# Optimization experiments

Hardware: AMD Instinct MI355X
Metric: run time of the kernel (lower is better)

The kernel has to match this reference:

```python
import jax, jax.numpy as jnp
import numpy as np

N = 6144
INPUT_SIZE = 1024
HIDDEN = 256
NEG_INF = -9e15  # matches torch masked_fill value -9000000000000000.0


def setup_inputs() -> dict:
    key = jax.random.key(0)
    k1, k2, k3, k4 = jax.random.split(key, 4)
    nodes_embed = jax.random.normal(k1, (N, INPUT_SIZE), dtype=jnp.float32)
    node_adj = jax.random.randint(k2, (N, N), 0, 2, dtype=jnp.int32)
    # learned params (xavier-uniform-ish scaling)
    limW = np.sqrt(6.0 / (INPUT_SIZE + HIDDEN))
    W = jax.random.uniform(k3, (INPUT_SIZE, HIDDEN), minval=-limW, maxval=limW, dtype=jnp.float32)
    lima = 1.414 * np.sqrt(6.0 / (2 * HIDDEN + 1))
    a_edge = jax.random.uniform(k4, (2 * HIDDEN,), minval=-lima, maxval=lima, dtype=jnp.float32)
    return {"nodes_embed": nodes_embed, "W": W, "a_edge": a_edge, "node_adj": node_adj}


def reference(nodes_embed, W, a_edge, node_adj):
    # h = nodes_embed @ W : [N, hidden]
    h = nodes_embed @ W
    # W_edge([h_i ; h_j]) decomposes exactly: (h_i @ a1) + (h_j @ a2)
    a1, a2 = a_edge[:HIDDEN], a_edge[HIDDEN:]
    score = (h @ a1)[:, None] + (h @ a2)[None, :]  # [N, N]
    adj_f = node_adj.astype(h.dtype)
    weight = jax.nn.leaky_relu(adj_f * score, negative_slope=0.2)
    weight = jnp.where(node_adj == 0, jnp.asarray(NEG_INF, h.dtype), weight)
    attention = jax.nn.softmax(weight, axis=-1)
    # dropout in eval mode (identity)
    return attention @ h  # [N, hidden]
```

## Files before the change

kernel.cpp:

```cpp
#include <hip/hip_runtime.h>
#include <hip/hip_bf16.h>

#define NN 6144
#define INPUT 1024
#define HID 256

using frag  = __attribute__((ext_vector_type(8))) short;
using f32x4 = __attribute__((ext_vector_type(4))) float;

static __device__ __forceinline__ unsigned short bf16u(float x) {
    unsigned u = __float_as_uint(x);
    u += 0x7fff + ((u >> 16) & 1);
    return (unsigned short)(u >> 16);
}

static __device__ __forceinline__ void lds_barrier() {
    asm volatile("s_waitcnt lgkmcnt(0)" ::: "memory");
    __builtin_amdgcn_s_barrier();
    __builtin_amdgcn_sched_barrier(0);
}

__global__ __launch_bounds__(256) void k_prep(const float* __restrict__ X,
                                              const float* __restrict__ W,
                                              unsigned short* __restrict__ Xb,
                                              unsigned short* __restrict__ Wt) {
    int b = blockIdx.x;
    if (b < 3072) {
        int t = b * 256 + threadIdx.x;
        const float4* p = reinterpret_cast<const float4*>(X) + (size_t)t * 2;
        float4 x0 = p[0], x1 = p[1];
        frag v;
        v[0] = (short)bf16u(x0.x); v[1] = (short)bf16u(x0.y);
        v[2] = (short)bf16u(x0.z); v[3] = (short)bf16u(x0.w);
        v[4] = (short)bf16u(x1.x); v[5] = (short)bf16u(x1.y);
        v[6] = (short)bf16u(x1.z); v[7] = (short)bf16u(x1.w);
        *reinterpret_cast<frag*>(Xb + (size_t)t * 8) = v;
    } else {
        int t = (b - 3072) * 256 + threadIdx.x;
        int n = t >> 10, k = t & 1023;
        Wt[t] = bf16u(W[k * HID + n]);
    }
}

__global__ __launch_bounds__(256) void k_gemm1(const unsigned short* __restrict__ Xb,
                                               const unsigned short* __restrict__ Wt,
                                               const float* __restrict__ a_edge,
                                               unsigned short* __restrict__ hT,
                                               float* __restrict__ s1,
                                               float* __restrict__ s2) {
    __shared__ unsigned short A[2][32][72];
    int t = threadIdx.x;
    int m = t >> 3, cg = t & 7;
    int i0 = blockIdx.x * 32, n0 = blockIdx.y * 64;
    int w = t >> 6, l = t & 63, lm = l & 15, q = l >> 4;
    int nw = n0 + w * 16;

    const unsigned short* xrow = Xb + (size_t)(i0 + m) * INPUT + cg * 8;
    const unsigned short* brow = Wt + (size_t)(nw + lm) * INPUT + q * 8;

    f32x4 acc0 = {}, acc1 = {};
    frag av = *reinterpret_cast<const frag*>(xrow);

    for (int c = 0; c < 16; c++) {
        int buf = c & 1;
        frag b0 = *reinterpret_cast<const frag*>(brow + c * 64);
        frag b1 = *reinterpret_cast<const frag*>(brow + c * 64 + 32);

        *reinterpret_cast<frag*>(&A[buf][m][cg * 8]) = av;
        if (c < 15) av = *reinterpret_cast<const frag*>(xrow + (c + 1) * 64);

        lds_barrier();

#pragma unroll
        for (int kk = 0; kk < 2; kk++) {
            frag a0 = *reinterpret_cast<const frag*>(&A[buf][lm][kk * 32 + q * 8]);
            frag a1 = *reinterpret_cast<const frag*>(&A[buf][16 + lm][kk * 32 + q * 8]);
            frag b  = kk ? b1 : b0;
            acc0 = __builtin_amdgcn_mfma_f32_16x16x32_bf16(a0, b, acc0, 0, 0, 0);
            acc1 = __builtin_amdgcn_mfma_f32_16x16x32_bf16(a1, b, acc1, 0, 0, 0);
        }
    }

    ushort4 o;
    o.x = bf16u(acc0[0]); o.y = bf16u(acc0[1]); o.z = bf16u(acc0[2]); o.w = bf16u(acc0[3]);
    *reinterpret_cast<ushort4*>(hT + (size_t)(nw + lm) * NN + i0 + q * 4) = o;
    o.x = bf16u(acc1[0]); o.y = bf16u(acc1[1]); o.z = bf16u(acc1[2]); o.w = bf16u(acc1[3]);
    *reinterpret_cast<ushort4*>(hT + (size_t)(nw + lm) * NN + i0 + 16 + q * 4) = o;

    float a1v = a_edge[nw + lm], a2v = a_edge[HID + nw + lm];
#pragma unroll
    for (int h = 0; h < 2; h++) {
        const f32x4& ac = h ? acc1 : acc0;
#pragma unroll
        for (int r = 0; r < 4; r++) {
            float v1 = ac[r] * a1v, v2 = ac[r] * a2v;
            v1 += __shfl_xor(v1, 1); v2 += __shfl_xor(v2, 1);
            v1 += __shfl_xor(v1, 2); v2 += __shfl_xor(v2, 2);
            v1 += __shfl_xor(v1, 4); v2 += __shfl_xor(v2, 4);
            v1 += __shfl_xor(v1, 8); v2 += __shfl_xor(v2, 8);
            if (lm == 0) {
                atomicAdd(&s1[i0 + h * 16 + q * 4 + r], v1);
                atomicAdd(&s2[i0 + h * 16 + q * 4 + r], v2);
            }
        }
    }
}

__global__ __launch_bounds__(512) void k_attn(const int* __restrict__ adj,
                                              const float* __restrict__ s1,
                                              const float* __restrict__ s2,
                                              const unsigned short* __restrict__ hT,
                                              float* __restrict__ U4,
                                              float* __restrict__ denom4) {
    __shared__ unsigned short P[2][32][136];
    int t = threadIdx.x;
    int m = t >> 4, cg = t & 15;
    int i0 = blockIdx.x * 32;
    int q4 = blockIdx.y;
    int j0 = q4 * 1536;
    int w = t >> 6, l = t & 63, lm = l & 15, q = l >> 4;

    float s1v = s1[i0 + m];
    const int*   arow = adj + (size_t)(i0 + m) * NN + j0 + cg * 8;
    const float* s2p  = s2 + j0 + cg * 8;

    const unsigned short* brow[2];
#pragma unroll
    for (int nt = 0; nt < 2; nt++)
        brow[nt] = hT + (size_t)(w * 32 + nt * 16 + lm) * NN + j0 + q * 8;

    f32x4 acc[2][2] = {};
    float dsum = 0.f;

    int4   ca0 = *reinterpret_cast<const int4*>(arow);
    int4   ca1 = *reinterpret_cast<const int4*>(arow + 4);
    float4 cs0 = *reinterpret_cast<const float4*>(s2p);
    float4 cs1 = *reinterpret_cast<const float4*>(s2p + 4);

    for (int c = 0; c < 12; c++) {
        int buf = c & 1;
        int jc = c * 128;

        frag bf[8];
#pragma unroll
        for (int kk = 0; kk < 4; kk++)
#pragma unroll
            for (int nt = 0; nt < 2; nt++)
                bf[kk * 2 + nt] = *reinterpret_cast<const frag*>(brow[nt] + jc + kk * 32);

        int4 na0 = {}, na1 = {};
        float4 ns0 = {}, ns1 = {};
        if (c < 11) {
            na0 = *reinterpret_cast<const int4*>(arow + jc + 128);
            na1 = *reinterpret_cast<const int4*>(arow + jc + 132);
            ns0 = *reinterpret_cast<const float4*>(s2p + jc + 128);
            ns1 = *reinterpret_cast<const float4*>(s2p + jc + 132);
        }

        float sc, wv, p0, p1, p2, p3, p4, p5, p6, p7;
        sc = s1v + cs0.x; wv = fmaxf(sc, 0.2f * sc); p0 = ca0.x ? __expf(wv) : 0.f;
        sc = s1v + cs0.y; wv = fmaxf(sc, 0.2f * sc); p1 = ca0.y ? __expf(wv) : 0.f;
        sc = s1v + cs0.z; wv = fmaxf(sc, 0.2f * sc); p2 = ca0.z ? __expf(wv) : 0.f;
        sc = s1v + cs0.w; wv = fmaxf(sc, 0.2f * sc); p3 = ca0.w ? __expf(wv) : 0.f;
        sc = s1v + cs1.x; wv = fmaxf(sc, 0.2f * sc); p4 = ca1.x ? __expf(wv) : 0.f;
        sc = s1v + cs1.y; wv = fmaxf(sc, 0.2f * sc); p5 = ca1.y ? __expf(wv) : 0.f;
        sc = s1v + cs1.z; wv = fmaxf(sc, 0.2f * sc); p6 = ca1.z ? __expf(wv) : 0.f;
        sc = s1v + cs1.w; wv = fmaxf(sc, 0.2f * sc); p7 = ca1.w ? __expf(wv) : 0.f;
        dsum += ((p0 + p1) + (p2 + p3)) + ((p4 + p5) + (p6 + p7));
        frag pk;
        pk[0] = (short)bf16u(p0); pk[1] = (short)bf16u(p1);
        pk[2] = (short)bf16u(p2); pk[3] = (short)bf16u(p3);
        pk[4] = (short)bf16u(p4); pk[5] = (short)bf16u(p5);
        pk[6] = (short)bf16u(p6); pk[7] = (short)bf16u(p7);
        *reinterpret_cast<frag*>(&P[buf][m][cg * 8]) = pk;

        lds_barrier();

        __builtin_amdgcn_s_setprio(1);
#pragma unroll
        for (int kk = 0; kk < 4; kk++) {
            frag a0 = *reinterpret_cast<const frag*>(&P[buf][lm][kk * 32 + q * 8]);
            frag a1 = *reinterpret_cast<const frag*>(&P[buf][16 + lm][kk * 32 + q * 8]);
#pragma unroll
            for (int nt = 0; nt < 2; nt++) {
                acc[0][nt] = __builtin_amdgcn_mfma_f32_16x16x32_bf16(a0, bf[kk * 2 + nt], acc[0][nt], 0, 0, 0);
                acc[1][nt] = __builtin_amdgcn_mfma_f32_16x16x32_bf16(a1, bf[kk * 2 + nt], acc[1][nt], 0, 0, 0);
            }
        }
        __builtin_amdgcn_s_setprio(0);

        ca0 = na0; ca1 = na1; cs0 = ns0; cs1 = ns1;
    }

    float v = dsum;
    v += __shfl_xor(v, 1); v += __shfl_xor(v, 2);
    v += __shfl_xor(v, 4); v += __shfl_xor(v, 8);
    if (cg == 0) denom4[(size_t)q4 * NN + i0 + m] = v;

    float* Ub = U4 + (size_t)q4 * NN * HID;
#pragma unroll
    for (int h = 0; h < 2; h++)
#pragma unroll
        for (int nt = 0; nt < 2; nt++)
#pragma unroll
            for (int r = 0; r < 4; r++)
                Ub[(size_t)(i0 + h * 16 + q * 4 + r) * HID + w * 32 + nt * 16 + lm] = acc[h][nt][r];
}

__global__ __launch_bounds__(256) void k_norm(const float* __restrict__ U4,
                                              const float* __restrict__ denom4,
                                              float* __restrict__ out) {
    int i = blockIdx.x, t = threadIdx.x;
    size_t S = (size_t)NN * HID;
    size_t base = (size_t)i * HID + t;
    float u = U4[base] + U4[base + S] + U4[base + 2 * S] + U4[base + 3 * S];
    float d = denom4[i] + denom4[i + NN] + denom4[i + 2 * NN] + denom4[i + 3 * NN];
    out[base] = (d != 0.f) ? u / d : 0.f;
}

extern "C" void kernel_launch(void* const* d_in, const int* in_sizes, int n_in,
                              void* d_out, int out_size, void* d_ws, size_t ws_size,
                              hipStream_t stream) {
    const float* X      = (const float*)d_in[0];
    const float* W      = (const float*)d_in[1];
    const float* a_edge = (const float*)d_in[2];
    const int*   adj    = (const int*)d_in[3];
    float* out = (float*)d_out;

    float* U4     = (float*)d_ws;
    float* denom4 = U4 + (size_t)4 * NN * HID;
    float* s1     = denom4 + (size_t)4 * NN;
    float* s2     = s1 + NN;
    unsigned short* hT = (unsigned short*)(s2 + NN);
    unsigned short* Wt = hT + (size_t)HID * NN;
    unsigned short* Xb = (unsigned short*)U4;

    hipMemsetAsync(s1, 0, 2 * NN * sizeof(float), stream);
    k_prep<<<3072 + INPUT * HID / 256, 256, 0, stream>>>(X, W, Xb, Wt);
    k_gemm1<<<dim3(NN / 32, HID / 64), 256, 0, stream>>>(Xb, Wt, a_edge, hT, s1, s2);
    k_attn<<<dim3(NN / 32, 4), 512, 0, stream>>>(adj, s1, s2, hT, U4, denom4);
    k_norm<<<NN, 256, 0, stream>>>(U4, denom4, out);
}
```

Measured before the change: 300.0 us.

## Drop LDS staging in projection GEMM, register-prefetch fragments, deepen attention adjacency prefetch

The projection GEMM now loads A and B MFMA fragments straight from global memory into double-buffered registers, with no LDS staging and no barriers. Each block runs 512 threads and covers 128 output columns. The attention kernel prefetches adjacency and s2 two chunks ahead instead of one, and both kernels get a launch-bounds occupancy hint of 4. The aim is to hide global latency better, at the cost of more registers and redundant global reads of X rows across waves.

```diff
diff --git a/kernel.cpp b/kernel.cpp
--- a/kernel.cpp
+++ b/kernel.cpp
@@ -42,52 +42,57 @@
     }
 }
 
-__global__ __launch_bounds__(256) void k_gemm1(const unsigned short* __restrict__ Xb,
-                                               const unsigned short* __restrict__ Wt,
-                                               const float* __restrict__ a_edge,
-                                               unsigned short* __restrict__ hT,
-                                               float* __restrict__ s1,
-                                               float* __restrict__ s2) {
-    __shared__ unsigned short A[2][32][72];
+__global__ __launch_bounds__(512, 4) void k_gemm1(const unsigned short* __restrict__ Xb,
+                                                  const unsigned short* __restrict__ Wt,
+                                                  const float* __restrict__ a_edge,
+                                                  unsigned short* __restrict__ hT,
+                                                  float* __restrict__ s1,
+                                                  float* __restrict__ s2) {
     int t = threadIdx.x;
-    int m = t >> 3, cg = t & 7;
-    int i0 = blockIdx.x * 32, n0 = blockIdx.y * 64;
+    int i0 = blockIdx.x * 32;
     int w = t >> 6, l = t & 63, lm = l & 15, q = l >> 4;
-    int nw = n0 + w * 16;
-
-    const unsigned short* xrow = Xb + (size_t)(i0 + m) * INPUT + cg * 8;
-    const unsigned short* brow = Wt + (size_t)(nw + lm) * INPUT + q * 8;
+    int n0 = blockIdx.y * 128 + w * 16;
+
+    const unsigned short* arow0 = Xb + (size_t)(i0 + lm) * INPUT + q * 8;
+    const unsigned short* arow1 = arow0 + 16 * INPUT;
+    const unsigned short* brow  = Wt + (size_t)(n0 + lm) * INPUT + q * 8;
 
     f32x4 acc0 = {}, acc1 = {};
-    frag av = *reinterpret_cast<const frag*>(xrow);
-
-    for (int c = 0; c < 16; c++) {
-        int buf = c & 1;
-        frag b0 = *reinterpret_cast<const frag*>(brow + c * 64);
-        frag b1 = *reinterpret_cast<const frag*>(brow + c * 64 + 32);
-
-        *reinterpret_cast<frag*>(&A[buf][m][cg * 8]) = av;
-        if (c < 15) av = *reinterpret_cast<const frag*>(xrow + (c + 1) * 64);
-
-        lds_barrier();
-
-#pragma unroll
-        for (int kk = 0; kk < 2; kk++) {
-            frag a0 = *reinterpret_cast<const frag*>(&A[buf][lm][kk * 32 + q * 8]);
-            frag a1 = *reinterpret_cast<const frag*>(&A[buf][16 + lm][kk * 32 + q * 8]);
-            frag b  = kk ? b1 : b0;
-            acc0 = __builtin_amdgcn_mfma_f32_16x16x32_bf16(a0, b, acc0, 0, 0, 0);
-            acc1 = __builtin_amdgcn_mfma_f32_16x16x32_bf16(a1, b, acc1, 0, 0, 0);
+
+    frag A0[2][4], A1[2][4], B[2][4];
+#pragma unroll
+    for (int j = 0; j < 4; j++) {
+        A0[0][j] = *reinterpret_cast<const frag*>(arow0 + j * 32);
+        A1[0][j] = *reinterpret_cast<const frag*>(arow1 + j * 32);
+        B[0][j]  = *reinterpret_cast<const frag*>(brow  + j * 32);
+    }
+
+#pragma unroll
+    for (int g = 0; g < 8; g++) {
+        int cur = g & 1, nxt = cur ^ 1;
+        if (g < 7) {
+#pragma unroll
+            for (int j = 0; j < 4; j++) {
+                int kk = (g + 1) * 4 + j;
+                A0[nxt][j] = *reinterpret_cast<const frag*>(arow0 + kk * 32);
+                A1[nxt][j] = *reinterpret_cast<const frag*>(arow1 + kk * 32);
+                B[nxt][j]  = *reinterpret_cast<const frag*>(brow  + kk * 32);
+            }
+        }
+#pragma unroll
+        for (int j = 0; j < 4; j++) {
+            acc0 = __builtin_amdgcn_mfma_f32_16x16x32_bf16(A0[cur][j], B[cur][j], acc0, 0, 0, 0);
+            acc1 = __builtin_amdgcn_mfma_f32_16x16x32_bf16(A1[cur][j], B[cur][j], acc1, 0, 0, 0);
         }
     }
 
     ushort4 o;
     o.x = bf16u(acc0[0]); o.y = bf16u(acc0[1]); o.z = bf16u(acc0[2]); o.w = bf16u(acc0[3]);
-    *reinterpret_cast<ushort4*>(hT + (size_t)(nw + lm) * NN + i0 + q * 4) = o;
+    *reinterpret_cast<ushort4*>(hT + (size_t)(n0 + lm) * NN + i0 + q * 4) = o;
     o.x = bf16u(acc1[0]); o.y = bf16u(acc1[1]); o.z = bf16u(acc1[2]); o.w = bf16u(acc1[3]);
-    *reinterpret_cast<ushort4*>(hT + (size_t)(nw + lm) * NN + i0 + 16 + q * 4) = o;
-
-    float a1v = a_edge[nw + lm], a2v = a_edge[HID + nw + lm];
+    *reinterpret_cast<ushort4*>(hT + (size_t)(n0 + lm) * NN + i0 + 16 + q * 4) = o;
+
+    float a1v = a_edge[n0 + lm], a2v = a_edge[HID + n0 + lm];
 #pragma unroll
     for (int h = 0; h < 2; h++) {
         const f32x4& ac = h ? acc1 : acc0;
@@ -106,12 +111,12 @@
     }
 }
 
-__global__ __launch_bounds__(512) void k_attn(const int* __restrict__ adj,
-                                              const float* __restrict__ s1,
-                                              const float* __restrict__ s2,
-                                              const unsigned short* __restrict__ hT,
-                                              float* __restrict__ U4,
-                                              float* __restrict__ denom4) {
+__global__ __launch_bounds__(512, 4) void k_attn(const int* __restrict__ adj,
+                                                 const float* __restrict__ s1,
+                                                 const float* __restrict__ s2,
+                                                 const unsigned short* __restrict__ hT,
+                                                 float* __restrict__ U4,
+                                                 float* __restrict__ denom4) {
     __shared__ unsigned short P[2][32][136];
     int t = threadIdx.x;
     int m = t >> 4, cg = t & 15;
@@ -136,6 +141,10 @@
     int4   ca1 = *reinterpret_cast<const int4*>(arow + 4);
     float4 cs0 = *reinterpret_cast<const float4*>(s2p);
     float4 cs1 = *reinterpret_cast<const float4*>(s2p + 4);
+    int4   na0 = *reinterpret_cast<const int4*>(arow + 128);
+    int4   na1 = *reinterpret_cast<const int4*>(arow + 132);
+    float4 ns0 = *reinterpret_cast<const float4*>(s2p + 128);
+    float4 ns1 = *reinterpret_cast<const float4*>(s2p + 132);
 
     for (int c = 0; c < 12; c++) {
         int buf = c & 1;
@@ -148,13 +157,13 @@
             for (int nt = 0; nt < 2; nt++)
                 bf[kk * 2 + nt] = *reinterpret_cast<const frag*>(brow[nt] + jc + kk * 32);
 
-        int4 na0 = {}, na1 = {};
-        float4 ns0 = {}, ns1 = {};
-        if (c < 11) {
-            na0 = *reinterpret_cast<const int4*>(arow + jc + 128);
-            na1 = *reinterpret_cast<const int4*>(arow + jc + 132);
-            ns0 = *reinterpret_cast<const float4*>(s2p + jc + 128);
-            ns1 = *reinterpret_cast<const float4*>(s2p + jc + 132);
+        int4 xa0 = {}, xa1 = {};
+        float4 xs0 = {}, xs1 = {};
+        if (c < 10) {
+            xa0 = *reinterpret_cast<const int4*>(arow + jc + 256);
+            xa1 = *reinterpret_cast<const int4*>(arow + jc + 260);
+            xs0 = *reinterpret_cast<const float4*>(s2p + jc + 256);
+            xs1 = *reinterpret_cast<const float4*>(s2p + jc + 260);
         }
 
         float sc, wv, p0, p1, p2, p3, p4, p5, p6, p7;
@@ -190,6 +199,7 @@
         __builtin_amdgcn_s_setprio(0);
 
         ca0 = na0; ca1 = na1; cs0 = ns0; cs1 = ns1;
+        na0 = xa0; na1 = xa1; ns0 = xs0; ns1 = xs1;
     }
 
     float v = dsum;
@@ -237,7 +247,7 @@
 
     hipMemsetAsync(s1, 0, 2 * NN * sizeof(float), stream);
     k_prep<<<3072 + INPUT * HID / 256, 256, 0, stream>>>(X, W, Xb, Wt);
-    k_gemm1<<<dim3(NN / 32, HID / 64), 256, 0, stream>>>(Xb, Wt, a_edge, hT, s1, s2);
+    k_gemm1<<<dim3(NN / 32, 2), 512, 0, stream>>>(Xb, Wt, a_edge, hT, s1, s2);
     k_attn<<<dim3(NN / 32, 4), 512, 0, stream>>>(adj, s1, s2, hT, U4, denom4);
     k_norm<<<NN, 256, 0, stream>>>(U4, denom4, out);
 }
```

After: 329.8 us. +9.9%, slower.

## Drop split-K in attention kernel, fuse normalization, and ping-pong register prefetch

Applied to the files above, without the earlier changes.

The attention kernel no longer splits the column range into four partial blocks. Each block now covers the full 6144 columns for its 32 rows and normalizes in-kernel through a shared-memory denominator, so the separate normalization kernel and the four partial U buffers go away. The loop is manually unrolled by two with alternating register sets for the B fragments and adjacency prefetch, and launch bounds request two blocks per CU. In exchange, the grid shrinks to 192 blocks, fewer than the CU count on MI355X, so parallelism and latency hiding may suffer.

```diff
diff --git a/kernel.cpp b/kernel.cpp
--- a/kernel.cpp
+++ b/kernel.cpp
@@ -106,116 +106,138 @@
     }
 }
 
-__global__ __launch_bounds__(512) void k_attn(const int* __restrict__ adj,
-                                              const float* __restrict__ s1,
-                                              const float* __restrict__ s2,
-                                              const unsigned short* __restrict__ hT,
-                                              float* __restrict__ U4,
-                                              float* __restrict__ denom4) {
+__global__ __launch_bounds__(512, 2) void k_attn(const int* __restrict__ adj,
+                                                 const float* __restrict__ s1,
+                                                 const float* __restrict__ s2,
+                                                 const unsigned short* __restrict__ hT,
+                                                 float* __restrict__ out) {
     __shared__ unsigned short P[2][32][136];
+    __shared__ float Dsm[32];
     int t = threadIdx.x;
     int m = t >> 4, cg = t & 15;
     int i0 = blockIdx.x * 32;
-    int q4 = blockIdx.y;
-    int j0 = q4 * 1536;
     int w = t >> 6, l = t & 63, lm = l & 15, q = l >> 4;
 
     float s1v = s1[i0 + m];
-    const int*   arow = adj + (size_t)(i0 + m) * NN + j0 + cg * 8;
-    const float* s2p  = s2 + j0 + cg * 8;
+    const int*   arow = adj + (size_t)(i0 + m) * NN + cg * 8;
+    const float* s2p  = s2 + cg * 8;
 
     const unsigned short* brow[2];
 #pragma unroll
     for (int nt = 0; nt < 2; nt++)
-        brow[nt] = hT + (size_t)(w * 32 + nt * 16 + lm) * NN + j0 + q * 8;
+        brow[nt] = hT + (size_t)(w * 32 + nt * 16 + lm) * NN + q * 8;
 
     f32x4 acc[2][2] = {};
     float dsum = 0.f;
 
-    int4   ca0 = *reinterpret_cast<const int4*>(arow);
-    int4   ca1 = *reinterpret_cast<const int4*>(arow + 4);
-    float4 cs0 = *reinterpret_cast<const float4*>(s2p);
-    float4 cs1 = *reinterpret_cast<const float4*>(s2p + 4);
-
-    for (int c = 0; c < 12; c++) {
-        int buf = c & 1;
-        int jc = c * 128;
-
-        frag bf[8];
-#pragma unroll
-        for (int kk = 0; kk < 4; kk++)
-#pragma unroll
-            for (int nt = 0; nt < 2; nt++)
-                bf[kk * 2 + nt] = *reinterpret_cast<const frag*>(brow[nt] + jc + kk * 32);
-
-        int4 na0 = {}, na1 = {};
-        float4 ns0 = {}, ns1 = {};
-        if (c < 11) {
-            na0 = *reinterpret_cast<const int4*>(arow + jc + 128);
-            na1 = *reinterpret_cast<const int4*>(arow + jc + 132);
-            ns0 = *reinterpret_cast<const float4*>(s2p + jc + 128);
-            ns1 = *reinterpret_cast<const float4*>(s2p + jc + 132);
-        }
-
-        float sc, wv, p0, p1, p2, p3, p4, p5, p6, p7;
-        sc = s1v + cs0.x; wv = fmaxf(sc, 0.2f * sc); p0 = ca0.x ? __expf(wv) : 0.f;
-        sc = s1v + cs0.y; wv = fmaxf(sc, 0.2f * sc); p1 = ca0.y ? __expf(wv) : 0.f;
-        sc = s1v + cs0.z; wv = fmaxf(sc, 0.2f * sc); p2 = ca0.z ? __expf(wv) : 0.f;
-        sc = s1v + cs0.w; wv = fmaxf(sc, 0.2f * sc); p3 = ca0.w ? __expf(wv) : 0.f;
-        sc = s1v + cs1.x; wv = fmaxf(sc, 0.2f * sc); p4 = ca1.x ? __expf(wv) : 0.f;
-        sc = s1v + cs1.y; wv = fmaxf(sc, 0.2f * sc); p5 = ca1.y ? __expf(wv) : 0.f;
-        sc = s1v + cs1.z; wv = fmaxf(sc, 0.2f * sc); p6 = ca1.z ? __expf(wv) : 0.f;
-        sc = s1v + cs1.w; wv = fmaxf(sc, 0.2f * sc); p7 = ca1.w ? __expf(wv) : 0.f;
-        dsum += ((p0 + p1) + (p2 + p3)) + ((p4 + p5) + (p6 + p7));
-        frag pk;
-        pk[0] = (short)bf16u(p0); pk[1] = (short)bf16u(p1);
-        pk[2] = (short)bf16u(p2); pk[3] = (short)bf16u(p3);
-        pk[4] = (short)bf16u(p4); pk[5] = (short)bf16u(p5);
-        pk[6] = (short)bf16u(p6); pk[7] = (short)bf16u(p7);
-        *reinterpret_cast<frag*>(&P[buf][m][cg * 8]) = pk;
-
-        lds_barrier();
-
-        __builtin_amdgcn_s_setprio(1);
-#pragma unroll
-        for (int kk = 0; kk < 4; kk++) {
-            frag a0 = *reinterpret_cast<const frag*>(&P[buf][lm][kk * 32 + q * 8]);
-            frag a1 = *reinterpret_cast<const frag*>(&P[buf][16 + lm][kk * 32 + q * 8]);
-#pragma unroll
-            for (int nt = 0; nt < 2; nt++) {
-                acc[0][nt] = __builtin_amdgcn_mfma_f32_16x16x32_bf16(a0, bf[kk * 2 + nt], acc[0][nt], 0, 0, 0);
-                acc[1][nt] = __builtin_amdgcn_mfma_f32_16x16x32_bf16(a1, bf[kk * 2 + nt], acc[1][nt], 0, 0, 0);
-            }
-        }
-        __builtin_amdgcn_s_setprio(0);
-
-        ca0 = na0; ca1 = na1; cs0 = ns0; cs1 = ns1;
-    }
+    int4   ea0 = *reinterpret_cast<const int4*>(arow);
+    int4   ea1 = *reinterpret_cast<const int4*>(arow + 4);
+    float4 es0 = *reinterpret_cast<const float4*>(s2p);
+    float4 es1 = *reinterpret_cast<const float4*>(s2p + 4);
+    int4   oa0 = *reinterpret_cast<const int4*>(arow + 128);
+    int4   oa1 = *reinterpret_cast<const int4*>(arow + 132);
+    float4 os0 = *reinterpret_cast<const float4*>(s2p + 128);
+    float4 os1 = *reinterpret_cast<const float4*>(s2p + 132);
+    frag bfA[8], bfB[8];
+#pragma unroll
+    for (int kk = 0; kk < 4; kk++)
+#pragma unroll
+        for (int nt = 0; nt < 2; nt++)
+            bfA[kk * 2 + nt] = *reinterpret_cast<const frag*>(brow[nt] + kk * 32);
+
+#define BUILD_P(A0, A1, S0, S1, PB)                                                   \
+    {                                                                                 \
+        float sc, wv, p0, p1, p2, p3, p4, p5, p6, p7;                                 \
+        sc = s1v + S0.x; wv = fmaxf(sc, 0.2f * sc); p0 = A0.x ? __expf(wv) : 0.f;     \
+        sc = s1v + S0.y; wv = fmaxf(sc, 0.2f * sc); p1 = A0.y ? __expf(wv) : 0.f;     \
+        sc = s1v + S0.z; wv = fmaxf(sc, 0.2f * sc); p2 = A0.z ? __expf(wv) : 0.f;     \
+        sc = s1v + S0.w; wv = fmaxf(sc, 0.2f * sc); p3 = A0.w ? __expf(wv) : 0.f;     \
+        sc = s1v + S1.x; wv = fmaxf(sc, 0.2f * sc); p4 = A1.x ? __expf(wv) : 0.f;     \
+        sc = s1v + S1.y; wv = fmaxf(sc, 0.2f * sc); p5 = A1.y ? __expf(wv) : 0.f;     \
+        sc = s1v + S1.z; wv = fmaxf(sc, 0.2f * sc); p6 = A1.z ? __expf(wv) : 0.f;     \
+        sc = s1v + S1.w; wv = fmaxf(sc, 0.2f * sc); p7 = A1.w ? __expf(wv) : 0.f;     \
+        dsum += ((p0 + p1) + (p2 + p3)) + ((p4 + p5) + (p6 + p7));                    \
+        frag pk;                                                                      \
+        pk[0] = (short)bf16u(p0); pk[1] = (short)bf16u(p1);                           \
+        pk[2] = (short)bf16u(p2); pk[3] = (short)bf16u(p3);                           \
+        pk[4] = (short)bf16u(p4); pk[5] = (short)bf16u(p5);                           \
+        pk[6] = (short)bf16u(p6); pk[7] = (short)bf16u(p7);                           \
+        *reinterpret_cast<frag*>(&P[PB][m][cg * 8]) = pk;                             \
+    }
+
+#define MFMA_P(PB, BF)                                                                \
+    __builtin_amdgcn_s_setprio(1);                                                    \
+    _Pragma("unroll")                                                                 \
+    for (int kk = 0; kk < 4; kk++) {                                                  \
+        frag a0 = *reinterpret_cast<const frag*>(&P[PB][lm][kk * 32 + q * 8]);        \
+        frag a1 = *reinterpret_cast<const frag*>(&P[PB][16 + lm][kk * 32 + q * 8]);   \
+        _Pragma("unroll")                                                             \
+        for (int nt = 0; nt < 2; nt++) {                                              \
+            acc[0][nt] = __builtin_amdgcn_mfma_f32_16x16x32_bf16(a0, BF[kk * 2 + nt], acc[0][nt], 0, 0, 0); \
+            acc[1][nt] = __builtin_amdgcn_mfma_f32_16x16x32_bf16(a1, BF[kk * 2 + nt], acc[1][nt], 0, 0, 0); \
+        }                                                                             \
+    }                                                                                 \
+    __builtin_amdgcn_s_setprio(0);
+
+    for (int c = 0; c < 48; c += 2) {
+        {
+            int jc = c * 128;
+            BUILD_P(ea0, ea1, es0, es1, 0)
+#pragma unroll
+            for (int kk = 0; kk < 4; kk++)
+#pragma unroll
+                for (int nt = 0; nt < 2; nt++)
+                    bfB[kk * 2 + nt] = *reinterpret_cast<const frag*>(brow[nt] + jc + 128 + kk * 32);
+            if (c + 2 < 48) {
+                ea0 = *reinterpret_cast<const int4*>(arow + jc + 256);
+                ea1 = *reinterpret_cast<const int4*>(arow + jc + 260);
+                es0 = *reinterpret_cast<const float4*>(s2p + jc + 256);
+                es1 = *reinterpret_cast<const float4*>(s2p + jc + 260);
+            }
+            lds_barrier();
+            MFMA_P(0, bfA)
+        }
+        {
+            int jc = c * 128 + 128;
+            BUILD_P(oa0, oa1, os0, os1, 1)
+            if (c + 2 < 48) {
+#pragma unroll
+                for (int kk = 0; kk < 4; kk++)
+#pragma unroll
+                    for (int nt = 0; nt < 2; nt++)
+                        bfA[kk * 2 + nt] = *reinterpret_cast<const frag*>(brow[nt] + jc + 128 + kk * 32);
+            }
+            if (c + 3 < 48) {
+                oa0 = *reinterpret_cast<const int4*>(arow + jc + 256);
+                oa1 = *reinterpret_cast<const int4*>(arow + jc + 260);
+                os0 = *reinterpret_cast<const float4*>(s2p + jc + 256);
+                os1 = *reinterpret_cast<const float4*>(s2p + jc + 260);
+            }
+            lds_barrier();
+            MFMA_P(1, bfB)
+        }
+    }
+#undef BUILD_P
+#undef MFMA_P
 
     float v = dsum;
     v += __shfl_xor(v, 1); v += __shfl_xor(v, 2);
     v += __shfl_xor(v, 4); v += __shfl_xor(v, 8);
-    if (cg == 0) denom4[(size_t)q4 * NN + i0 + m] = v;
-
-    float* Ub = U4 + (size_t)q4 * NN * HID;
+    if (cg == 0) Dsm[m] = v;
+    __syncthreads();
+
+    float* orow = out + (size_t)i0 * HID;
 #pragma unroll
     for (int h = 0; h < 2; h++)
 #pragma unroll
         for (int nt = 0; nt < 2; nt++)
 #pragma unroll
-            for (int r = 0; r < 4; r++)
-                Ub[(size_t)(i0 + h * 16 + q * 4 + r) * HID + w * 32 + nt * 16 + lm] = acc[h][nt][r];
-}
-
-__global__ __launch_bounds__(256) void k_norm(const float* __restrict__ U4,
-                                              const float* __restrict__ denom4,
-                                              float* __restrict__ out) {
-    int i = blockIdx.x, t = threadIdx.x;
-    size_t S = (size_t)NN * HID;
-    size_t base = (size_t)i * HID + t;
-    float u = U4[base] + U4[base + S] + U4[base + 2 * S] + U4[base + 3 * S];
-    float d = denom4[i] + denom4[i + NN] + denom4[i + 2 * NN] + denom4[i + 3 * NN];
-    out[base] = (d != 0.f) ? u / d : 0.f;
+            for (int r = 0; r < 4; r++) {
+                int row = h * 16 + q * 4 + r;
+                float d = Dsm[row];
+                float val = (d != 0.f) ? acc[h][nt][r] / d : 0.f;
+                orow[(size_t)row * HID + w * 32 + nt * 16 + lm] = val;
+            }
 }
 
 extern "C" void kernel_launch(void* const* d_in, const int* in_sizes, int n_in,
@@ -227,17 +249,14 @@
     const int*   adj    = (const int*)d_in[3];
     float* out = (float*)d_out;
 
-    float* U4     = (float*)d_ws;
-    float* denom4 = U4 + (size_t)4 * NN * HID;
-    float* s1     = denom4 + (size_t)4 * NN;
-    float* s2     = s1 + NN;
+    float* s1 = (float*)d_ws;
+    float* s2 = s1 + NN;
     unsigned short* hT = (unsigned short*)(s2 + NN);
     unsigned short* Wt = hT + (size_t)HID * NN;
-    unsigned short* Xb = (unsigned short*)U4;
+    unsigned short* Xb = Wt + (size_t)HID * INPUT;
 
     hipMemsetAsync(s1, 0, 2 * NN * sizeof(float), stream);
     k_prep<<<3072 + INPUT * HID / 256, 256, 0, stream>>>(X, W, Xb, Wt);
     k_gemm1<<<dim3(NN / 32, HID / 64), 256, 0, stream>>>(Xb, Wt, a_edge, hT, s1, s2);
-    k_attn<<<dim3(NN / 32, 4), 512, 0, stream>>>(adj, s1, s2, hT, U4, denom4);
-    k_norm<<<NN, 256, 0, stream>>>(U4, denom4, out);
-}
+    k_attn<<<NN / 32, 512, 0, stream>>>(adj, s1, s2, hT, out);
+}
```

Result: slower. 321.1 us (+7.0%).

## Stage X and adjacency tiles via global_load_lds double buffering with swizzle

Applied to the files above, without the earlier changes.

Both the first GEMM and the attention kernel now load their streamed tiles (X rows, adjacency, s2) directly into LDS with the asynchronous global_load_lds builtin. Double buffering is driven by vmcnt waits and barriers instead of register prefetch followed by LDS stores. GEMM1 doubles its K chunk to 128, uses an XOR swizzle to avoid LDS bank conflicts, and adds occupancy hints to the launch bounds. The goal is to cut register pressure and VGPR-to-LDS store traffic and to overlap loads with compute, at the cost of more LDS use and a fragile vmcnt-based synchronisation.

```diff
diff --git a/kernel.cpp b/kernel.cpp
--- a/kernel.cpp
+++ b/kernel.cpp
@@ -12,6 +12,15 @@
     unsigned u = __float_as_uint(x);
     u += 0x7fff + ((u >> 16) & 1);
     return (unsigned short)(u >> 16);
+}
+
+static __device__ __forceinline__ void gll16(const void* g, void* l) {
+    __builtin_amdgcn_global_load_lds((__attribute__((address_space(1))) const void*)g,
+                                     (__attribute__((address_space(3))) void*)l, 16, 0, 0);
+}
+static __device__ __forceinline__ void gll4(const void* g, void* l) {
+    __builtin_amdgcn_global_load_lds((__attribute__((address_space(1))) const void*)g,
+                                     (__attribute__((address_space(3))) void*)l, 4, 0, 0);
 }
 
 static __device__ __forceinline__ void lds_barrier() {
@@ -42,44 +51,53 @@
     }
 }
 
-__global__ __launch_bounds__(256) void k_gemm1(const unsigned short* __restrict__ Xb,
-                                               const unsigned short* __restrict__ Wt,
-                                               const float* __restrict__ a_edge,
-                                               unsigned short* __restrict__ hT,
-                                               float* __restrict__ s1,
-                                               float* __restrict__ s2) {
-    __shared__ unsigned short A[2][32][72];
+__global__ __launch_bounds__(256, 4) void k_gemm1(const unsigned short* __restrict__ Xb,
+                                                  const unsigned short* __restrict__ Wt,
+                                                  const float* __restrict__ a_edge,
+                                                  unsigned short* __restrict__ hT,
+                                                  float* __restrict__ s1,
+                                                  float* __restrict__ s2) {
+    __shared__ unsigned short A[2][32][128];
     int t = threadIdx.x;
-    int m = t >> 3, cg = t & 7;
     int i0 = blockIdx.x * 32, n0 = blockIdx.y * 64;
     int w = t >> 6, l = t & 63, lm = l & 15, q = l >> 4;
     int nw = n0 + w * 16;
 
-    const unsigned short* xrow = Xb + (size_t)(i0 + m) * INPUT + cg * 8;
     const unsigned short* brow = Wt + (size_t)(nw + lm) * INPUT + q * 8;
 
+    int r0 = w * 8 + (l >> 4);
+    const unsigned short* xs0 = Xb + (size_t)(i0 + r0) * INPUT + (((l & 15) ^ (r0 & 7)) << 3);
+    const unsigned short* xs1 = Xb + (size_t)(i0 + r0 + 4) * INPUT + (((l & 15) ^ ((r0 + 4) & 7)) << 3);
+
+#define GSTAGE(C, BUF) { \
+        gll16(xs0 + (C) * 128, &A[BUF][w * 8][0]); \
+        gll16(xs1 + (C) * 128, &A[BUF][w * 8 + 4][0]); }
+
     f32x4 acc0 = {}, acc1 = {};
-    frag av = *reinterpret_cast<const frag*>(xrow);
-
-    for (int c = 0; c < 16; c++) {
+    GSTAGE(0, 0)
+
+    for (int c = 0; c < 8; c++) {
         int buf = c & 1;
-        frag b0 = *reinterpret_cast<const frag*>(brow + c * 64);
-        frag b1 = *reinterpret_cast<const frag*>(brow + c * 64 + 32);
-
-        *reinterpret_cast<frag*>(&A[buf][m][cg * 8]) = av;
-        if (c < 15) av = *reinterpret_cast<const frag*>(xrow + (c + 1) * 64);
-
-        lds_barrier();
-
-#pragma unroll
-        for (int kk = 0; kk < 2; kk++) {
-            frag a0 = *reinterpret_cast<const frag*>(&A[buf][lm][kk * 32 + q * 8]);
-            frag a1 = *reinterpret_cast<const frag*>(&A[buf][16 + lm][kk * 32 + q * 8]);
-            frag b  = kk ? b1 : b0;
+        frag b0 = *reinterpret_cast<const frag*>(brow + c * 128);
+        frag b1 = *reinterpret_cast<const frag*>(brow + c * 128 + 32);
+        frag b2 = *reinterpret_cast<const frag*>(brow + c * 128 + 64);
+        frag b3 = *reinterpret_cast<const frag*>(brow + c * 128 + 96);
+        asm volatile("s_waitcnt vmcnt(4)" ::: "memory");
+        __builtin_amdgcn_s_barrier();
+        __builtin_amdgcn_sched_barrier(0);
+        if (c < 7) GSTAGE(c + 1, buf ^ 1)
+
+#pragma unroll
+        for (int kk = 0; kk < 4; kk++) {
+            int sw = (kk * 32 + q * 8) ^ ((lm & 7) << 3);
+            frag a0 = *reinterpret_cast<const frag*>(&A[buf][lm][sw]);
+            frag a1 = *reinterpret_cast<const frag*>(&A[buf][16 + lm][sw]);
+            frag b  = (kk == 0) ? b0 : (kk == 1) ? b1 : (kk == 2) ? b2 : b3;
             acc0 = __builtin_amdgcn_mfma_f32_16x16x32_bf16(a0, b, acc0, 0, 0, 0);
             acc1 = __builtin_amdgcn_mfma_f32_16x16x32_bf16(a1, b, acc1, 0, 0, 0);
         }
     }
+#undef GSTAGE
 
     ushort4 o;
     o.x = bf16u(acc0[0]); o.y = bf16u(acc0[1]); o.z = bf16u(acc0[2]); o.w = bf16u(acc0[3]);
@@ -106,23 +124,24 @@
     }
 }
 
-__global__ __launch_bounds__(512) void k_attn(const int* __restrict__ adj,
-                                              const float* __restrict__ s1,
-                                              const float* __restrict__ s2,
-                                              const unsigned short* __restrict__ hT,
-                                              float* __restrict__ U4,
-                                              float* __restrict__ denom4) {
+__global__ __launch_bounds__(512, 2) void k_attn(const int* __restrict__ adj,
+                                                 const float* __restrict__ s1,
+                                                 const float* __restrict__ s2,
+                                                 const unsigned short* __restrict__ hT,
+                                                 float* __restrict__ U4,
+                                                 float* __restrict__ denom4) {
     __shared__ unsigned short P[2][32][136];
+    __shared__ int   adjS[2][32][128];
+    __shared__ float s2S[2][128];
     int t = threadIdx.x;
     int m = t >> 4, cg = t & 15;
     int i0 = blockIdx.x * 32;
-    int q4 = blockIdx.y;
-    int j0 = q4 * 1536;
+    int q4 = blockIdx.y, j0 = q4 * 1536;
     int w = t >> 6, l = t & 63, lm = l & 15, q = l >> 4;
 
     float s1v = s1[i0 + m];
-    const int*   arow = adj + (size_t)(i0 + m) * NN + j0 + cg * 8;
-    const float* s2p  = s2 + j0 + cg * 8;
+    const int*   astage = adj + (size_t)(i0 + w * 4 + (l >> 5)) * NN + j0 + (l & 31) * 4;
+    const float* sstage = s2 + j0 + w * 16 + l;
 
     const unsigned short* brow[2];
 #pragma unroll
@@ -132,14 +151,15 @@
     f32x4 acc[2][2] = {};
     float dsum = 0.f;
 
-    int4   ca0 = *reinterpret_cast<const int4*>(arow);
-    int4   ca1 = *reinterpret_cast<const int4*>(arow + 4);
-    float4 cs0 = *reinterpret_cast<const float4*>(s2p);
-    float4 cs1 = *reinterpret_cast<const float4*>(s2p + 4);
+#define STAGE(JC, BUF) { \
+        gll16(astage + (JC), &adjS[BUF][w * 4][0]); \
+        gll16(astage + (JC) + 2 * NN, &adjS[BUF][w * 4 + 2][0]); \
+        if (l < 16) gll4(sstage + (JC), &s2S[BUF][w * 16]); }
+
+    STAGE(0, 0)
 
     for (int c = 0; c < 12; c++) {
-        int buf = c & 1;
-        int jc = c * 128;
+        int buf = c & 1, jc = c * 128;
 
         frag bf[8];
 #pragma unroll
@@ -148,31 +168,35 @@
             for (int nt = 0; nt < 2; nt++)
                 bf[kk * 2 + nt] = *reinterpret_cast<const frag*>(brow[nt] + jc + kk * 32);
 
-        int4 na0 = {}, na1 = {};
-        float4 ns0 = {}, ns1 = {};
-        if (c < 11) {
-            na0 = *reinterpret_cast<const int4*>(arow + jc + 128);
-            na1 = *reinterpret_cast<const int4*>(arow + jc + 132);
-            ns0 = *reinterpret_cast<const float4*>(s2p + jc + 128);
-            ns1 = *reinterpret_cast<const float4*>(s2p + jc + 132);
-        }
-
-        float sc, wv, p0, p1, p2, p3, p4, p5, p6, p7;
-        sc = s1v + cs0.x; wv = fmaxf(sc, 0.2f * sc); p0 = ca0.x ? __expf(wv) : 0.f;
-        sc = s1v + cs0.y; wv = fmaxf(sc, 0.2f * sc); p1 = ca0.y ? __expf(wv) : 0.f;
-        sc = s1v + cs0.z; wv = fmaxf(sc, 0.2f * sc); p2 = ca0.z ? __expf(wv) : 0.f;
-        sc = s1v + cs0.w; wv = fmaxf(sc, 0.2f * sc); p3 = ca0.w ? __expf(wv) : 0.f;
-        sc = s1v + cs1.x; wv = fmaxf(sc, 0.2f * sc); p4 = ca1.x ? __expf(wv) : 0.f;
-        sc = s1v + cs1.y; wv = fmaxf(sc, 0.2f * sc); p5 = ca1.y ? __expf(wv) : 0.f;
-        sc = s1v + cs1.z; wv = fmaxf(sc, 0.2f * sc); p6 = ca1.z ? __expf(wv) : 0.f;
-        sc = s1v + cs1.w; wv = fmaxf(sc, 0.2f * sc); p7 = ca1.w ? __expf(wv) : 0.f;
-        dsum += ((p0 + p1) + (p2 + p3)) + ((p4 + p5) + (p6 + p7));
-        frag pk;
-        pk[0] = (short)bf16u(p0); pk[1] = (short)bf16u(p1);
-        pk[2] = (short)bf16u(p2); pk[3] = (short)bf16u(p3);
-        pk[4] = (short)bf16u(p4); pk[5] = (short)bf16u(p5);
-        pk[6] = (short)bf16u(p6); pk[7] = (short)bf16u(p7);
-        *reinterpret_cast<frag*>(&P[buf][m][cg * 8]) = pk;
+        asm volatile("s_waitcnt vmcnt(8)" ::: "memory");
+        __builtin_amdgcn_s_barrier();
+        __builtin_amdgcn_sched_barrier(0);
+        if (c < 11) STAGE(jc + 128, buf ^ 1)
+
+        {
+            const int*   aL = &adjS[buf][m][cg * 8];
+            const float* sL = &s2S[buf][cg * 8];
+            int4   av0 = *reinterpret_cast<const int4*>(aL);
+            int4   av1 = *reinterpret_cast<const int4*>(aL + 4);
+            float4 sv0 = *reinterpret_cast<const float4*>(sL);
+            float4 sv1 = *reinterpret_cast<const float4*>(sL + 4);
+            float sc, wv, p0, p1, p2, p3, p4, p5, p6, p7;
+            sc = s1v + sv0.x; wv = fmaxf(sc, 0.2f * sc); p0 = av0.x ? __expf(wv) : 0.f;
+            sc = s1v + sv0.y; wv = fmaxf(sc, 0.2f * sc); p1 = av0.y ? __expf(wv) : 0.f;
+            sc = s1v + sv0.z; wv = fmaxf(sc, 0.2f * sc); p2 = av0.z ? __expf(wv) : 0.f;
+            sc = s1v + sv0.w; wv = fmaxf(sc, 0.2f * sc); p3 = av0.w ? __expf(wv) : 0.f;
+            sc = s1v + sv1.x; wv = fmaxf(sc, 0.2f * sc); p4 = av1.x ? __expf(wv) : 0.f;
+            sc = s1v + sv1.y; wv = fmaxf(sc, 0.2f * sc); p5 = av1.y ? __expf(wv) : 0.f;
+            sc = s1v + sv1.z; wv = fmaxf(sc, 0.2f * sc); p6 = av1.z ? __expf(wv) : 0.f;
+            sc = s1v + sv1.w; wv = fmaxf(sc, 0.2f * sc); p7 = av1.w ? __expf(wv) : 0.f;
+            dsum += ((p0 + p1) + (p2 + p3)) + ((p4 + p5) + (p6 + p7));
+            frag pk;
+            pk[0] = (short)bf16u(p0); pk[1] = (short)bf16u(p1);
+            pk[2] = (short)bf16u(p2); pk[3] = (short)bf16u(p3);
+            pk[4] = (short)bf16u(p4); pk[5] = (short)bf16u(p5);
+            pk[6] = (short)bf16u(p6); pk[7] = (short)bf16u(p7);
+            *reinterpret_cast<frag*>(&P[buf][m][cg * 8]) = pk;
+        }
 
         lds_barrier();
 
@@ -188,9 +212,8 @@
             }
         }
         __builtin_amdgcn_s_setprio(0);
-
-        ca0 = na0; ca1 = na1; cs0 = ns0; cs1 = ns1;
-    }
+    }
+#undef STAGE
 
     float v = dsum;
     v += __shfl_xor(v, 1); v += __shfl_xor(v, 2);
```

New measurement: 307.2 us. 2.4% more time.
